# Performance work log

Hardware: AMD Instinct MI355X
Metric: run time of the kernel (lower is better)

Reference implementation:

```python
import jax, jax.numpy as jnp
import numpy as np

B, SEQ, S, DIM_IN, DIM_K, DIM_V = 4, 2048, 128, 512, 64, 64
L = SEQ + 2 * S
NEG = -1e30  # stand-in for log(0) in the tril mask (finite for stable vjp)


def _layernorm(x, g, b, eps=1e-5):
    m = jnp.mean(x, axis=-1, keepdims=True)
    v = jnp.var(x, axis=-1, keepdims=True)
    return (x - m) / jnp.sqrt(v + eps) * g + b


def setup_inputs() -> dict:
    key = jax.random.key(0)
    ks = jax.random.split(key, 18)
    w = lambda k, shape, s=0.02: (jax.random.normal(k, shape, jnp.float32) * s)
    inp = {
        "x": jax.random.normal(ks[0], (B, L, DIM_IN), jnp.float32),
        "Wq": w(ks[1], (DIM_IN, DIM_K)),
        "Wk": w(ks[2], (DIM_IN, DIM_K)),
        "Wv": w(ks[3], (DIM_IN, DIM_V)),
        "Wq_s": w(ks[4], (DIM_IN, DIM_K)),
        "Wk_s": w(ks[5], (DIM_IN, DIM_K)),
        "Wv_s": w(ks[6], (DIM_IN, DIM_V)),
        "Wq_e": w(ks[7], (DIM_IN, DIM_K)),
        "Wk_e": w(ks[8], (DIM_IN, DIM_K)),
        "Wv_e": w(ks[9], (DIM_IN, DIM_V)),
        "ln_g": jnp.ones((DIM_IN,), jnp.float32),
        "ln_b": jnp.zeros((DIM_IN,), jnp.float32),
        "ln_s_g": jnp.ones((DIM_IN,), jnp.float32),
        "ln_s_b": jnp.zeros((DIM_IN,), jnp.float32),
        "ln_e_g": jnp.ones((DIM_IN,), jnp.float32),
        "ln_e_b": jnp.zeros((DIM_IN,), jnp.float32),
        "cope_emb": jax.random.normal(ks[10], (DIM_K, S), jnp.float32),
        "offset": 0,
    }
    return inp


def reference(x, Wq, Wk, Wv, Wq_s, Wk_s, Wv_s, Wq_e, Wk_e, Wv_e,
              ln_g, ln_b, ln_s_g, ln_s_b, ln_e_g, ln_e_b, cope_emb, offset):
    # extract_state: first/last state_len tokens
    xs, xm, xe = x[:, :S], x[:, S:L - S], x[:, -S:]
    xm = _layernorm(xm, ln_g, ln_b)
    xs = _layernorm(xs, ln_s_g, ln_s_b)
    xe = _layernorm(xe, ln_e_g, ln_e_b)

    q, k, v = xm @ Wq, xm @ Wk, xm @ Wv          # (B, SEQ, dk/dv)
    q_s, k_s, v_s = xs @ Wq_s, xs @ Wk_s, xs @ Wv_s
    q_e, k_e, v_e = xe @ Wq_e, xe @ Wk_e, xe @ Wv_e

    # CoPE bias over the non-state block
    logits = jnp.einsum('bqd,bkd->bqk', q, k)    # (B, SEQ, SEQ)
    gates = jax.nn.sigmoid(logits)
    pos = jnp.flip(jnp.cumsum(jnp.flip(gates, -1), axis=-1), -1)
    pos = jnp.minimum(pos, jnp.float32(S - 1))
    pos_ceil = jnp.ceil(pos).astype(jnp.int32)
    pos_floor = jnp.floor(pos).astype(jnp.int32)
    logits_int = jnp.einsum('bqd,dk->bqk', q, cope_emb)  # (B, SEQ, S)
    logits_c = jnp.take_along_axis(logits_int, pos_ceil, axis=-1)
    logits_f = jnp.take_along_axis(logits_int, pos_floor, axis=-1)
    wfrac = pos - pos_floor.astype(pos.dtype)
    bias = logits_c * wfrac + logits_f * (1.0 - wfrac)   # (B, SEQ, SEQ)

    q_full = jnp.concatenate([q_s, q, q_e], axis=1)      # (B, L, dk)
    k_full = jnp.concatenate([k_s, k, k_e], axis=1)
    v_full = jnp.concatenate([v_s, v, v_e], axis=1)

    # explicit tril log-mask bias with CoPE injected in the middle block
    tri = jnp.tril(jnp.ones((L, L), dtype=bool))
    attn_bias = jnp.where(tri, 0.0, NEG).astype(jnp.float32)
    attn_bias = jnp.broadcast_to(attn_bias, (B, L, L))
    attn_bias = attn_bias.at[:, S:L - S, S:L - S].add(bias)

    scale = 1.0 / jnp.sqrt(jnp.float32(DIM_K))
    scores = jnp.einsum('bqd,bkd->bqk', q_full, k_full) * scale + attn_bias
    att = jax.nn.softmax(scores, axis=-1)
    return jnp.einsum('bqk,bkd->bqd', att, v_full)       # (B, L, dv)
```

## Files before the change

kernel.cpp:

```cpp
#include <hip/hip_runtime.h>
#include <math.h>

#define B_    4
#define SEQ_  2048
#define S_    128
#define L_    2304
#define DIN   512
#define DK    64
#define NEGINF (-1e30f)
#define SCALE 0.125f
#define NCOLS 2176
#define NMID  8192
#define NEDGE 1024
#define LE    2304

typedef _Float16 f16;
typedef __attribute__((ext_vector_type(8))) _Float16 half8;
typedef __attribute__((ext_vector_type(4))) float f32x4;

union U4 { uint4 u; f16 h[8]; };

__global__ __launch_bounds__(256) void k_proj(
    const float* __restrict__ x,
    const float* __restrict__ Wq,  const float* __restrict__ Wk,  const float* __restrict__ Wv,
    const float* __restrict__ Wqs, const float* __restrict__ Wks, const float* __restrict__ Wvs,
    const float* __restrict__ Wqe, const float* __restrict__ Wke, const float* __restrict__ Wve,
    const float* __restrict__ g0, const float* __restrict__ b0,
    const float* __restrict__ gs, const float* __restrict__ bs,
    const float* __restrict__ ge, const float* __restrict__ be,
    f16* __restrict__ qsp, f16* __restrict__ ksp, f16* __restrict__ vhT)
{
    __shared__ f16 As[64 * 136];
    __shared__ f16 Bs[64 * 136];
    __shared__ float mean_s[64], rstd_s[64];
    const int tid  = threadIdx.x;
    const int row0 = blockIdx.x * 64;
    const int rseq = row0 % L_;
    const int seg  = (rseq < S_) ? 0 : (rseq >= L_ - S_) ? 2 : 1;
    const int m    = blockIdx.y;
    const float* W;
    if (m == 0)      W = (seg == 0) ? Wqs : (seg == 2) ? Wqe : Wq;
    else if (m == 1) W = (seg == 0) ? Wks : (seg == 2) ? Wke : Wk;
    else             W = (seg == 0) ? Wvs : (seg == 2) ? Wve : Wv;
    const float* gg = (seg == 0) ? gs : (seg == 2) ? ge : g0;
    const float* bb = (seg == 0) ? bs : (seg == 2) ? be : b0;

    {
        const int rr = tid >> 2, qq = tid & 3;
        const float4* xr = (const float4*)(x + (size_t)(row0 + rr) * DIN) + qq * 32;
        float s = 0.f, s2 = 0.f;
        #pragma unroll
        for (int i = 0; i < 32; ++i) {
            float4 v = xr[i];
            s  += v.x + v.y + v.z + v.w;
            s2 += v.x * v.x + v.y * v.y + v.z * v.z + v.w * v.w;
        }
        s  += __shfl_xor(s, 1);  s  += __shfl_xor(s, 2);
        s2 += __shfl_xor(s2, 1); s2 += __shfl_xor(s2, 2);
        if (qq == 0) {
            float mean = s * (1.f / DIN);
            mean_s[rr] = mean;
            rstd_s[rr] = rsqrtf(s2 * (1.f / DIN) - mean * mean + 1e-5f);
        }
    }

    const int w = tid >> 6, lane = tid & 63;
    const int cl = lane & 15, quad = lane >> 4;
    const int r0 = 32 * (w >> 1), c0 = 32 * (w & 1);

    f32x4 acc[2][2];
    #pragma unroll
    for (int i = 0; i < 2; ++i)
        #pragma unroll
        for (int j = 0; j < 2; ++j) acc[i][j] = 0.f;

    for (int kc = 0; kc < DIN; kc += 64) {
        __syncthreads();
        #pragma unroll
        for (int i = 0; i < 2; ++i) {
            int g = tid + 256 * i;
            int r = g >> 3, c8 = g & 7;
            const float* xp = x + (size_t)(row0 + r) * DIN + kc + c8 * 8;
            float4 a0 = *(const float4*)xp;
            float4 a1 = *(const float4*)(xp + 4);
            float4 gA = *(const float4*)(gg + kc + c8 * 8);
            float4 gB = *(const float4*)(gg + kc + c8 * 8 + 4);
            float4 bA = *(const float4*)(bb + kc + c8 * 8);
            float4 bB = *(const float4*)(bb + kc + c8 * 8 + 4);
            float mean = mean_s[r], rstd = rstd_s[r];
            float n[8];
            n[0] = (a0.x - mean) * rstd * gA.x + bA.x;
            n[1] = (a0.y - mean) * rstd * gA.y + bA.y;
            n[2] = (a0.z - mean) * rstd * gA.z + bA.z;
            n[3] = (a0.w - mean) * rstd * gA.w + bA.w;
            n[4] = (a1.x - mean) * rstd * gB.x + bB.x;
            n[5] = (a1.y - mean) * rstd * gB.y + bB.y;
            n[6] = (a1.z - mean) * rstd * gB.z + bB.z;
            n[7] = (a1.w - mean) * rstd * gB.w + bB.w;
            U4 hi, lo;
            #pragma unroll
            for (int j = 0; j < 8; ++j) {
                hi.h[j] = (f16)n[j];
                lo.h[j] = (f16)(n[j] - (float)hi.h[j]);
            }
            *(uint4*)(As + r * 136 + c8 * 8)      = hi.u;
            *(uint4*)(As + r * 136 + 64 + c8 * 8) = lo.u;
        }
        #pragma unroll
        for (int i = 0; i < 4; ++i) {
            int g = tid + 256 * i;
            int k = g >> 4, c4 = g & 15;
            float4 wv = ((const float4*)W)[(size_t)(kc + k) * 16 + c4];
            f16 h0 = (f16)wv.x, h1 = (f16)wv.y, h2 = (f16)wv.z, h3 = (f16)wv.w;
            Bs[(c4 * 4 + 0) * 136 + k] = h0;
            Bs[(c4 * 4 + 1) * 136 + k] = h1;
            Bs[(c4 * 4 + 2) * 136 + k] = h2;
            Bs[(c4 * 4 + 3) * 136 + k] = h3;
            Bs[(c4 * 4 + 0) * 136 + 64 + k] = (f16)(wv.x - (float)h0);
            Bs[(c4 * 4 + 1) * 136 + 64 + k] = (f16)(wv.y - (float)h1);
            Bs[(c4 * 4 + 2) * 136 + 64 + k] = (f16)(wv.z - (float)h2);
            Bs[(c4 * 4 + 3) * 136 + 64 + k] = (f16)(wv.w - (float)h3);
        }
        __syncthreads();
        #pragma unroll
        for (int h = 0; h < 2; ++h) {
            half8 ah[2], al[2], bh[2], bl[2];
            #pragma unroll
            for (int rs = 0; rs < 2; ++rs) {
                const f16* base = As + (r0 + 16 * rs + cl) * 136 + h * 32 + quad * 8;
                ah[rs] = *(const half8*)(base);
                al[rs] = *(const half8*)(base + 64);
            }
            #pragma unroll
            for (int cs = 0; cs < 2; ++cs) {
                const f16* base = Bs + (c0 + 16 * cs + cl) * 136 + h * 32 + quad * 8;
                bh[cs] = *(const half8*)(base);
                bl[cs] = *(const half8*)(base + 64);
            }
            #pragma unroll
            for (int rs = 0; rs < 2; ++rs)
                #pragma unroll
                for (int cs = 0; cs < 2; ++cs) {
                    acc[rs][cs] = __builtin_amdgcn_mfma_f32_16x16x32_f16(ah[rs], bh[cs], acc[rs][cs], 0, 0, 0);
                    if (m < 2) {
                        acc[rs][cs] = __builtin_amdgcn_mfma_f32_16x16x32_f16(ah[rs], bl[cs], acc[rs][cs], 0, 0, 0);
                        acc[rs][cs] = __builtin_amdgcn_mfma_f32_16x16x32_f16(al[rs], bh[cs], acc[rs][cs], 0, 0, 0);
                    }
                }
        }
    }

    const int bI = row0 / L_;
    const int rb = row0 - bI * L_;
    f16* sp = (m == 0) ? qsp : ksp;
    #pragma unroll
    for (int rs = 0; rs < 2; ++rs)
        #pragma unroll
        for (int cs = 0; cs < 2; ++cs)
            #pragma unroll
            for (int r = 0; r < 4; ++r) {
                int lrow = r0 + 16 * rs + quad * 4 + r;
                int col  = c0 + 16 * cs + cl;
                float v  = acc[rs][cs][r];
                size_t grow = (size_t)(row0 + lrow);
                if (m < 2) {
                    f16 hv = (f16)v;
                    sp[grow * 128 + col]      = hv;
                    sp[grow * 128 + 64 + col] = (f16)(v - (float)hv);
                } else {
                    vhT[(size_t)(bI * 64 + col) * L_ + rb + lrow] = (f16)v;
                }
            }
}

__global__ __launch_bounds__(256) void k_dots(
    const f16* __restrict__ qsp, const f16* __restrict__ ksp,
    f16* __restrict__ D, float* __restrict__ G, f16* __restrict__ De)
{
    const int bx = blockIdx.x, by = blockIdx.y;
    const bool edge = (bx >= 64);
    int b, q0 = 0;
    size_t qrow0;
    if (!edge) {
        if (by >= 34) return;
        b = bx >> 4;
        q0 = (bx * 128) & 2047;
        qrow0 = (size_t)b * L_ + S_ + q0;
    } else {
        int ex = bx - 64;
        b = ex >> 1;
        int half = ex & 1;
        if (half == 0 && by > 1) return;
        qrow0 = (size_t)b * L_ + (half ? 2176 : 0);
    }
    const int col0 = by * 64;
    const size_t krow0 = (size_t)b * L_ + col0;

    __shared__ f16 Qs[128 * 136];
    __shared__ f16 Ks[64 * 136];
    const int tid = threadIdx.x;

    #pragma unroll
    for (int i = 0; i < 8; ++i) {
        int g = tid + 256 * i;
        int r = g >> 4, c = g & 15;
        *(uint4*)(Qs + r * 136 + c * 8) = *(const uint4*)(qsp + (qrow0 + r) * 128 + c * 8);
    }
    #pragma unroll
    for (int i = 0; i < 4; ++i) {
        int g = tid + 256 * i;
        int r = g >> 4, c = g & 15;
        *(uint4*)(Ks + r * 136 + c * 8) = *(const uint4*)(ksp + (krow0 + r) * 128 + c * 8);
    }
    __syncthreads();

    const int w = tid >> 6, lane = tid & 63;
    const int cl = lane & 15, quad = lane >> 4;

    f32x4 acc[2][4];
    #pragma unroll
    for (int i = 0; i < 2; ++i)
        #pragma unroll
        for (int j = 0; j < 4; ++j) acc[i][j] = 0.f;

    #pragma unroll
    for (int h = 0; h < 2; ++h) {
        half8 ah[2], al[2], bh[4], bl[4];
        #pragma unroll
        for (int rs = 0; rs < 2; ++rs) {
            const f16* base = Qs + (32 * w + 16 * rs + cl) * 136 + h * 32 + quad * 8;
            ah[rs] = *(const half8*)(base);
            al[rs] = *(const half8*)(base + 64);
        }
        #pragma unroll
        for (int c = 0; c < 4; ++c) {
            const f16* base = Ks + (16 * c + cl) * 136 + h * 32 + quad * 8;
            bh[c] = *(const half8*)(base);
            bl[c] = *(const half8*)(base + 64);
        }
        #pragma unroll
        for (int rs = 0; rs < 2; ++rs)
            #pragma unroll
            for (int c = 0; c < 4; ++c) {
                acc[rs][c] = __builtin_amdgcn_mfma_f32_16x16x32_f16(ah[rs], bh[c], acc[rs][c], 0, 0, 0);
                acc[rs][c] = __builtin_amdgcn_mfma_f32_16x16x32_f16(ah[rs], bl[c], acc[rs][c], 0, 0, 0);
                acc[rs][c] = __builtin_amdgcn_mfma_f32_16x16x32_f16(al[rs], bh[c], acc[rs][c], 0, 0, 0);
            }
    }

    if (!edge) {
        const int gr0 = bx * 128;
        const bool writeD = (by < 2) || ((by - 2) <= (q0 >> 6) + 1);
        if (writeD) {
            #pragma unroll
            for (int rs = 0; rs < 2; ++rs)
                #pragma unroll
                for (int c = 0; c < 4; ++c)
                    #pragma unroll
                    for (int r = 0; r < 4; ++r) {
                        int mrow = gr0 + 32 * w + 16 * rs + quad * 4 + r;
                        int n    = col0 + 16 * c + cl;
                        D[(size_t)mrow * NCOLS + n] = (f16)acc[rs][c][r];
                    }
        }
        if (by >= 2) {
            const int chm = by - 2;
            #pragma unroll
            for (int rs = 0; rs < 2; ++rs)
                #pragma unroll
                for (int r = 0; r < 4; ++r) {
                    float s = 0.f;
                    #pragma unroll
                    for (int c = 0; c < 4; ++c)
                        s += 1.f / (1.f + __expf(-acc[rs][c][r]));
                    #pragma unroll
                    for (int off = 1; off < 16; off <<= 1) s += __shfl_xor(s, off);
                    if (cl == 0)
                        G[(size_t)(gr0 + 32 * w + 16 * rs + quad * 4 + r) * 32 + chm] = s;
                }
        }
    } else {
        const int er0 = (bx - 64) * 128;
        #pragma unroll
        for (int rs = 0; rs < 2; ++rs)
            #pragma unroll
            for (int c = 0; c < 4; ++c)
                #pragma unroll
                for (int r = 0; r < 4; ++r) {
                    int erow = er0 + 32 * w + 16 * rs + quad * 4 + r;
                    int n    = col0 + 16 * c + cl;
                    De[(size_t)erow * LE + n] = (f16)acc[rs][c][r];
                }
    }
}

__global__ __launch_bounds__(256) void k_scan(
    const f16* __restrict__ qsp, const float* __restrict__ cope,
    const float* __restrict__ G, f16* __restrict__ D, f16* __restrict__ De)
{
    __shared__ f16   qvh[128];
    __shared__ float li[128];
    __shared__ float Gs[32];
    __shared__ float Gsf[32];
    __shared__ float wmax[4], wsum[4];
    const int tid = threadIdx.x;
    const int gr  = blockIdx.x;
    const int lane = tid & 63, wid = tid >> 6;

    if (gr < NMID) {
        const int b = gr >> 11;
        const int q = gr & 2047;
        const size_t grow = (size_t)b * L_ + S_ + q;
        const int qlim = (q & ~63) + 64;

        if (tid < 16) ((uint4*)qvh)[tid] = ((const uint4*)(qsp + grow * 128))[tid];
        if (tid >= 16 && tid < 24)
            ((float4*)Gs)[tid - 16] = ((const float4*)G)[(size_t)gr * 8 + tid - 16];
        __syncthreads();
        if (tid < 128) {
            float a = 0.f;
            #pragma unroll
            for (int d = 0; d < DK; ++d)
                a += ((float)qvh[d] + (float)qvh[64 + d]) * cope[d * S_ + tid];
            li[tid] = a;
        }
        if (tid >= 128 && tid < 160) {
            int c = tid - 128;
            float s = 0.f;
            for (int cc = c + 1; cc < 32; ++cc) s += Gs[cc];
            Gsf[c] = s;
        }

        f16* Dr = D + (size_t)gr * NCOLS;
        const int j0 = tid * 8;
        const int cg = tid >> 3, sl = tid & 7;
        float dot[8], gte[8];
        float csum = 0.f;
        if (j0 < qlim) {
            U4 t; t.u = *(const uint4*)(Dr + 128 + j0);
            #pragma unroll
            for (int jj = 0; jj < 8; ++jj) {
                dot[jj] = (float)t.h[jj];
                gte[jj] = 1.f / (1.f + __expf(-dot[jj]));
                csum += gte[jj];
            }
        } else {
            #pragma unroll
            for (int jj = 0; jj < 8; ++jj) { dot[jj] = 0.f; gte[jj] = 0.f; }
        }
        float sv = (tid < 128) ? (float)Dr[tid] * SCALE : NEGINF;

        float inc = csum;
        #pragma unroll
        for (int off = 1; off < 8; off <<= 1) {
            float u = __shfl_down(inc, off, 8);
            if (sl + off < 8) inc += u;
        }
        __syncthreads();
        float run = (inc - csum) + Gsf[cg];

        float p8[8];
        #pragma unroll
        for (int jj = 7; jj >= 0; --jj) {
            run += gte[jj];
            float pos = fminf(run, (float)(S_ - 1));
            float pfl = floorf(pos);
            int ic  = (int)ceilf(pos);
            int ifl = (int)pfl;
            float w = pos - pfl;
            float bias = li[ic] * w + li[ifl] * (1.f - w);
            p8[jj] = (j0 + jj <= q) ? dot[jj] * SCALE + bias : NEGINF;
        }

        float mx = sv;
        #pragma unroll
        for (int jj = 0; jj < 8; ++jj) mx = fmaxf(mx, p8[jj]);
        #pragma unroll
        for (int off = 1; off < 64; off <<= 1) mx = fmaxf(mx, __shfl_xor(mx, off));
        if (lane == 0) wmax[wid] = mx;
        __syncthreads();
        mx = fmaxf(fmaxf(wmax[0], wmax[1]), fmaxf(wmax[2], wmax[3]));

        float lsum = 0.f;
        float e8[8];
        #pragma unroll
        for (int jj = 0; jj < 8; ++jj) {
            e8[jj] = __expf(p8[jj] - mx);
            lsum += e8[jj];
        }
        float es = 0.f;
        if (tid < 128) { es = __expf(sv - mx); lsum += es; }
        #pragma unroll
        for (int off = 1; off < 64; off <<= 1) lsum += __shfl_xor(lsum, off);
        if (lane == 0) wsum[wid] = lsum;
        __syncthreads();
        float inv = 1.f / (wsum[0] + wsum[1] + wsum[2] + wsum[3]);

        if (j0 < qlim) {
            U4 o;
            #pragma unroll
            for (int jj = 0; jj < 8; ++jj) o.h[jj] = (f16)(e8[jj] * inv);
            *(uint4*)(Dr + 128 + j0) = o.u;
        }
        if (tid < 128) Dr[tid] = (f16)(es * inv);
    } else {
        const int er = gr - NMID;
        const int r  = er & 255;
        const int Q  = (r < 128) ? r : (2048 + r);
        f16* Er = De + (size_t)er * LE;

        float v[9];
        #pragma unroll
        for (int i = 0; i < 9; ++i) {
            int j = tid + 256 * i;
            float d = (float)Er[j];
            v[i] = (j <= Q) ? d * SCALE : NEGINF;
        }
        float mx = v[0];
        #pragma unroll
        for (int i = 1; i < 9; ++i) mx = fmaxf(mx, v[i]);
        #pragma unroll
        for (int off = 1; off < 64; off <<= 1) mx = fmaxf(mx, __shfl_xor(mx, off));
        if (lane == 0) wmax[wid] = mx;
        __syncthreads();
        mx = fmaxf(fmaxf(wmax[0], wmax[1]), fmaxf(wmax[2], wmax[3]));

        float lsum = 0.f;
        #pragma unroll
        for (int i = 0; i < 9; ++i) {
            v[i] = __expf(v[i] - mx);
            lsum += v[i];
        }
        #pragma unroll
        for (int off = 1; off < 64; off <<= 1) lsum += __shfl_xor(lsum, off);
        if (lane == 0) wsum[wid] = lsum;
        __syncthreads();
        float inv = 1.f / (wsum[0] + wsum[1] + wsum[2] + wsum[3]);

        #pragma unroll
        for (int i = 0; i < 9; ++i)
            Er[tid + 256 * i] = (f16)(v[i] * inv);
    }
}

__global__ __launch_bounds__(256) void k_pv(
    const f16* __restrict__ Pmid, const f16* __restrict__ Pedge,
    const f16* __restrict__ vhT, float* __restrict__ out)
{
    __shared__ f16 Ps[64 * 72];
    __shared__ f16 Vt[64 * 72];
    const int tid = threadIdx.x;
    const int bx  = blockIdx.x;
    const int ks  = blockIdx.y;
    const bool edge = (bx >= 128);

    const f16* Pb;
    size_t pitch;
    int row0, b, cap, cmax;
    if (!edge) {
        row0 = bx * 64;
        b = row0 >> 11;
        int q0 = row0 & 2047;
        Pb = Pmid; pitch = NCOLS; cap = 34;
        cmax = (191 + q0) >> 6;
    } else {
        row0 = (bx - 128) * 64;
        b = row0 >> 8;
        int r0 = row0 & 255;
        Pb = Pedge; pitch = LE; cap = 36;
        int Qmax = (r0 < 128) ? (r0 + 63) : (2048 + r0 + 63);
        cmax = Qmax >> 6;
    }
    const int c_beg = ks * 9;
    int c_end = c_beg + 9;
    if (c_end > cap) c_end = cap;
    if (c_end > cmax + 1) c_end = cmax + 1;
    if (c_end <= c_beg) return;

    const int w = tid >> 6, lane = tid & 63;
    const int cl = lane & 15, quad = lane >> 4;
    f32x4 acc[4];
    #pragma unroll
    for (int c = 0; c < 4; ++c) acc[c] = 0.f;

    for (int ch = c_beg; ch < c_end; ++ch) {
        __syncthreads();
        #pragma unroll
        for (int i = 0; i < 2; ++i) {
            int g = tid + 256 * i;
            int r = g >> 3, c = g & 7;
            *(uint4*)(Ps + r * 72 + c * 8) =
                *(const uint4*)(Pb + (size_t)(row0 + r) * pitch + ch * 64 + c * 8);
            *(uint4*)(Vt + r * 72 + c * 8) =
                *(const uint4*)(vhT + (size_t)(b * 64 + r) * L_ + ch * 64 + c * 8);
        }
        __syncthreads();
        #pragma unroll
        for (int h = 0; h < 2; ++h) {
            half8 a = *(const half8*)(Ps + (16 * w + cl) * 72 + h * 32 + quad * 8);
            #pragma unroll
            for (int c = 0; c < 4; ++c) {
                half8 bv = *(const half8*)(Vt + (16 * c + cl) * 72 + h * 32 + quad * 8);
                acc[c] = __builtin_amdgcn_mfma_f32_16x16x32_f16(a, bv, acc[c], 0, 0, 0);
            }
        }
    }
    #pragma unroll
    for (int c = 0; c < 4; ++c)
        #pragma unroll
        for (int r = 0; r < 4; ++r) {
            int lrow = row0 + 16 * w + quad * 4 + r;
            int n    = 16 * c + cl;
            size_t orow;
            if (!edge) {
                orow = (size_t)b * L_ + S_ + (lrow & 2047);
            } else {
                int rr = lrow & 255;
                int gQ = (rr < 128) ? rr : (2048 + rr);
                orow = (size_t)b * L_ + gQ;
            }
            atomicAdd(&out[orow * DK + n], acc[c][r]);
        }
}

extern "C" void kernel_launch(void* const* d_in, const int* in_sizes, int n_in,
                              void* d_out, int out_size, void* d_ws, size_t ws_size,
                              hipStream_t stream)
{
    const float* x    = (const float*)d_in[0];
    const float* Wq   = (const float*)d_in[1];
    const float* Wk   = (const float*)d_in[2];
    const float* Wv   = (const float*)d_in[3];
    const float* Wqs  = (const float*)d_in[4];
    const float* Wks  = (const float*)d_in[5];
    const float* Wvs  = (const float*)d_in[6];
    const float* Wqe  = (const float*)d_in[7];
    const float* Wke  = (const float*)d_in[8];
    const float* Wve  = (const float*)d_in[9];
    const float* g0   = (const float*)d_in[10];
    const float* b0   = (const float*)d_in[11];
    const float* gs   = (const float*)d_in[12];
    const float* bs   = (const float*)d_in[13];
    const float* ge   = (const float*)d_in[14];
    const float* be   = (const float*)d_in[15];
    const float* cope = (const float*)d_in[16];

    const size_t NR = (size_t)B_ * L_;
    f16*   qsp = (f16*)d_ws;
    f16*   ksp = qsp + NR * 128;
    f16*   vhT = ksp + NR * 128;
    float* G   = (float*)(vhT + NR * 64);
    f16*   D   = (f16*)(G + (size_t)NMID * 32);
    f16*   De  = D + (size_t)NMID * NCOLS;
    float* out = (float*)d_out;

    hipMemsetAsync(out, 0, (size_t)out_size * sizeof(float), stream);
    k_proj<<<dim3(144, 3), 256, 0, stream>>>(x, Wq, Wk, Wv, Wqs, Wks, Wvs,
                                             Wqe, Wke, Wve, g0, b0, gs, bs,
                                             ge, be, qsp, ksp, vhT);
    k_dots<<<dim3(72, 36), 256, 0, stream>>>(qsp, ksp, D, G, De);
    k_scan<<<NMID + NEDGE, 256, 0, stream>>>(qsp, cope, G, D, De);
    k_pv  <<<dim3(144, 4), 256, 0, stream>>>(D, De, vhT, out);
}
```

Measured before the change: 199.2 us.

## Presplit weights, widen dots tile, replace PV atomics with partial-sum merge

Adds a kernel that converts and transposes each weight matrix into hi/lo fp16 pairs once, so the projection blocks stop redoing that conversion with scattered LDS stores. The dots kernel now computes 128-column key tiles instead of 64, halving the number of blocks and Q reloads, and emits two gate-sum chunks per block. The PV kernel writes per-split partial outputs to a workspace and a new merge kernel sums them, replacing the memset and the float atomics. This costs two extra launches, more workspace traffic, and more accumulator registers in the dots kernel.

Result: faster. 192.5 us (-3.4%).

```diff
diff --git a/kernel.cpp b/kernel.cpp
--- a/kernel.cpp
+++ b/kernel.cpp
@@ -20,11 +20,49 @@
 
 union U4 { uint4 u; f16 h[8]; };
 
-__global__ __launch_bounds__(256) void k_proj(
-    const float* __restrict__ x,
+__global__ __launch_bounds__(256) void k_wsplit(
     const float* __restrict__ Wq,  const float* __restrict__ Wk,  const float* __restrict__ Wv,
     const float* __restrict__ Wqs, const float* __restrict__ Wks, const float* __restrict__ Wvs,
     const float* __restrict__ Wqe, const float* __restrict__ Wke, const float* __restrict__ Wve,
+    f16* __restrict__ Wsp)
+{
+    __shared__ float xs[64 * 68];
+    const int kt  = blockIdx.x;
+    const int mat = blockIdx.y;
+    const float* W;
+    switch (mat) {
+        case 0: W = Wq;  break; case 1: W = Wk;  break; case 2: W = Wv;  break;
+        case 3: W = Wqs; break; case 4: W = Wks; break; case 5: W = Wvs; break;
+        case 6: W = Wqe; break; case 7: W = Wke; break; default: W = Wve; break;
+    }
+    const int tid = threadIdx.x;
+    const int k0  = kt * 64;
+    #pragma unroll
+    for (int i = 0; i < 4; ++i) {
+        int g = tid + 256 * i;
+        int k = g >> 4, c4 = g & 15;
+        *(float4*)(xs + k * 68 + c4 * 4) = ((const float4*)W)[(size_t)(k0 + k) * 16 + c4];
+    }
+    __syncthreads();
+    const int col = tid & 63, hf = tid >> 6;
+    const int kk0 = hf * 16;
+    U4 hi0, hi1, lo0, lo1;
+    #pragma unroll
+    for (int j = 0; j < 8; ++j) {
+        float v0 = xs[(kk0 + j) * 68 + col];
+        float v1 = xs[(kk0 + 8 + j) * 68 + col];
+        hi0.h[j] = (f16)v0; lo0.h[j] = (f16)(v0 - (float)hi0.h[j]);
+        hi1.h[j] = (f16)v1; lo1.h[j] = (f16)(v1 - (float)hi1.h[j]);
+    }
+    f16* dst = Wsp + (size_t)mat * 65536 + (size_t)col * 1024 + k0 + kk0;
+    *(uint4*)(dst)       = hi0.u;
+    *(uint4*)(dst + 8)   = hi1.u;
+    *(uint4*)(dst + 512) = lo0.u;
+    *(uint4*)(dst + 520) = lo1.u;
+}
+
+__global__ __launch_bounds__(256) void k_proj(
+    const float* __restrict__ x, const f16* __restrict__ Wsp,
     const float* __restrict__ g0, const float* __restrict__ b0,
     const float* __restrict__ gs, const float* __restrict__ bs,
     const float* __restrict__ ge, const float* __restrict__ be,
@@ -38,10 +76,8 @@
     const int rseq = row0 % L_;
     const int seg  = (rseq < S_) ? 0 : (rseq >= L_ - S_) ? 2 : 1;
     const int m    = blockIdx.y;
-    const float* W;
-    if (m == 0)      W = (seg == 0) ? Wqs : (seg == 2) ? Wqe : Wq;
-    else if (m == 1) W = (seg == 0) ? Wks : (seg == 2) ? Wke : Wk;
-    else             W = (seg == 0) ? Wvs : (seg == 2) ? Wve : Wv;
+    const int mat  = m + ((seg == 0) ? 3 : (seg == 2) ? 6 : 0);
+    const f16* Wc  = Wsp + (size_t)mat * 65536;
     const float* gg = (seg == 0) ? gs : (seg == 2) ? ge : g0;
     const float* bb = (seg == 0) ? bs : (seg == 2) ? be : b0;
 
@@ -107,19 +143,12 @@
             *(uint4*)(As + r * 136 + 64 + c8 * 8) = lo.u;
         }
         #pragma unroll
-        for (int i = 0; i < 4; ++i) {
+        for (int i = 0; i < 2; ++i) {
             int g = tid + 256 * i;
-            int k = g >> 4, c4 = g & 15;
-            float4 wv = ((const float4*)W)[(size_t)(kc + k) * 16 + c4];
-            f16 h0 = (f16)wv.x, h1 = (f16)wv.y, h2 = (f16)wv.z, h3 = (f16)wv.w;
-            Bs[(c4 * 4 + 0) * 136 + k] = h0;
-            Bs[(c4 * 4 + 1) * 136 + k] = h1;
-            Bs[(c4 * 4 + 2) * 136 + k] = h2;
-            Bs[(c4 * 4 + 3) * 136 + k] = h3;
-            Bs[(c4 * 4 + 0) * 136 + 64 + k] = (f16)(wv.x - (float)h0);
-            Bs[(c4 * 4 + 1) * 136 + 64 + k] = (f16)(wv.y - (float)h1);
-            Bs[(c4 * 4 + 2) * 136 + 64 + k] = (f16)(wv.z - (float)h2);
-            Bs[(c4 * 4 + 3) * 136 + 64 + k] = (f16)(wv.w - (float)h3);
+            int col = g >> 3, c8 = g & 7;
+            const f16* src = Wc + (size_t)col * 1024 + kc + c8 * 8;
+            *(uint4*)(Bs + col * 136 + c8 * 8)      = *(const uint4*)(src);
+            *(uint4*)(Bs + col * 136 + 64 + c8 * 8) = *(const uint4*)(src + 512);
         }
         __syncthreads();
         #pragma unroll
@@ -182,7 +211,7 @@
     int b, q0 = 0;
     size_t qrow0;
     if (!edge) {
-        if (by >= 34) return;
+        if (by >= 17) return;
         b = bx >> 4;
         q0 = (bx * 128) & 2047;
         qrow0 = (size_t)b * L_ + S_ + q0;
@@ -190,14 +219,14 @@
         int ex = bx - 64;
         b = ex >> 1;
         int half = ex & 1;
-        if (half == 0 && by > 1) return;
+        if (half == 0 && by > 0) return;
         qrow0 = (size_t)b * L_ + (half ? 2176 : 0);
     }
-    const int col0 = by * 64;
+    const int col0 = by * 128;
     const size_t krow0 = (size_t)b * L_ + col0;
 
     __shared__ f16 Qs[128 * 136];
-    __shared__ f16 Ks[64 * 136];
+    __shared__ f16 Ks[128 * 136];
     const int tid = threadIdx.x;
 
     #pragma unroll
@@ -205,11 +234,6 @@
         int g = tid + 256 * i;
         int r = g >> 4, c = g & 15;
         *(uint4*)(Qs + r * 136 + c * 8) = *(const uint4*)(qsp + (qrow0 + r) * 128 + c * 8);
-    }
-    #pragma unroll
-    for (int i = 0; i < 4; ++i) {
-        int g = tid + 256 * i;
-        int r = g >> 4, c = g & 15;
         *(uint4*)(Ks + r * 136 + c * 8) = *(const uint4*)(ksp + (krow0 + r) * 128 + c * 8);
     }
     __syncthreads();
@@ -217,15 +241,15 @@
     const int w = tid >> 6, lane = tid & 63;
     const int cl = lane & 15, quad = lane >> 4;
 
-    f32x4 acc[2][4];
+    f32x4 acc[2][8];
     #pragma unroll
     for (int i = 0; i < 2; ++i)
         #pragma unroll
-        for (int j = 0; j < 4; ++j) acc[i][j] = 0.f;
+        for (int j = 0; j < 8; ++j) acc[i][j] = 0.f;
 
     #pragma unroll
     for (int h = 0; h < 2; ++h) {
-        half8 ah[2], al[2], bh[4], bl[4];
+        half8 ah[2], al[2];
         #pragma unroll
         for (int rs = 0; rs < 2; ++rs) {
             const f16* base = Qs + (32 * w + 16 * rs + cl) * 136 + h * 32 + quad * 8;
@@ -233,29 +257,34 @@
             al[rs] = *(const half8*)(base + 64);
         }
         #pragma unroll
-        for (int c = 0; c < 4; ++c) {
-            const f16* base = Ks + (16 * c + cl) * 136 + h * 32 + quad * 8;
-            bh[c] = *(const half8*)(base);
-            bl[c] = *(const half8*)(base + 64);
-        }
-        #pragma unroll
-        for (int rs = 0; rs < 2; ++rs)
-            #pragma unroll
-            for (int c = 0; c < 4; ++c) {
-                acc[rs][c] = __builtin_amdgcn_mfma_f32_16x16x32_f16(ah[rs], bh[c], acc[rs][c], 0, 0, 0);
-                acc[rs][c] = __builtin_amdgcn_mfma_f32_16x16x32_f16(ah[rs], bl[c], acc[rs][c], 0, 0, 0);
-                acc[rs][c] = __builtin_amdgcn_mfma_f32_16x16x32_f16(al[rs], bh[c], acc[rs][c], 0, 0, 0);
+        for (int cq = 0; cq < 2; ++cq) {
+            half8 bh[4], bl[4];
+            #pragma unroll
+            for (int cc = 0; cc < 4; ++cc) {
+                const f16* base = Ks + (16 * (cq * 4 + cc) + cl) * 136 + h * 32 + quad * 8;
+                bh[cc] = *(const half8*)(base);
+                bl[cc] = *(const half8*)(base + 64);
             }
+            #pragma unroll
+            for (int rs = 0; rs < 2; ++rs)
+                #pragma unroll
+                for (int cc = 0; cc < 4; ++cc) {
+                    int c = cq * 4 + cc;
+                    acc[rs][c] = __builtin_amdgcn_mfma_f32_16x16x32_f16(ah[rs], bh[cc], acc[rs][c], 0, 0, 0);
+                    acc[rs][c] = __builtin_amdgcn_mfma_f32_16x16x32_f16(ah[rs], bl[cc], acc[rs][c], 0, 0, 0);
+                    acc[rs][c] = __builtin_amdgcn_mfma_f32_16x16x32_f16(al[rs], bh[cc], acc[rs][c], 0, 0, 0);
+                }
+        }
     }
 
     if (!edge) {
         const int gr0 = bx * 128;
-        const bool writeD = (by < 2) || ((by - 2) <= (q0 >> 6) + 1);
+        const bool writeD = (by == 0) || ((by - 1) <= (q0 >> 7));
         if (writeD) {
             #pragma unroll
             for (int rs = 0; rs < 2; ++rs)
                 #pragma unroll
-                for (int c = 0; c < 4; ++c)
+                for (int c = 0; c < 8; ++c)
                     #pragma unroll
                     for (int r = 0; r < 4; ++r) {
                         int mrow = gr0 + 32 * w + 16 * rs + quad * 4 + r;
@@ -263,20 +292,28 @@
                         D[(size_t)mrow * NCOLS + n] = (f16)acc[rs][c][r];
                     }
         }
-        if (by >= 2) {
-            const int chm = by - 2;
+        if (by >= 1) {
+            const int chm = 2 * (by - 1);
             #pragma unroll
             for (int rs = 0; rs < 2; ++rs)
                 #pragma unroll
                 for (int r = 0; r < 4; ++r) {
-                    float s = 0.f;
+                    float sA = 0.f, sB = 0.f;
                     #pragma unroll
-                    for (int c = 0; c < 4; ++c)
-                        s += 1.f / (1.f + __expf(-acc[rs][c][r]));
+                    for (int cc = 0; cc < 4; ++cc) {
+                        sA += 1.f / (1.f + __expf(-acc[rs][cc][r]));
+                        sB += 1.f / (1.f + __expf(-acc[rs][4 + cc][r]));
+                    }
                     #pragma unroll
-                    for (int off = 1; off < 16; off <<= 1) s += __shfl_xor(s, off);
-                    if (cl == 0)
-                        G[(size_t)(gr0 + 32 * w + 16 * rs + quad * 4 + r) * 32 + chm] = s;
+                    for (int off = 1; off < 16; off <<= 1) {
+                        sA += __shfl_xor(sA, off);
+                        sB += __shfl_xor(sB, off);
+                    }
+                    if (cl == 0) {
+                        int row = gr0 + 32 * w + 16 * rs + quad * 4 + r;
+                        G[(size_t)row * 32 + chm]     = sA;
+                        G[(size_t)row * 32 + chm + 1] = sB;
+                    }
                 }
         }
     } else {
@@ -284,7 +321,7 @@
         #pragma unroll
         for (int rs = 0; rs < 2; ++rs)
             #pragma unroll
-            for (int c = 0; c < 4; ++c)
+            for (int c = 0; c < 8; ++c)
                 #pragma unroll
                 for (int r = 0; r < 4; ++r) {
                     int erow = er0 + 32 * w + 16 * rs + quad * 4 + r;
@@ -445,7 +482,8 @@
 
 __global__ __launch_bounds__(256) void k_pv(
     const f16* __restrict__ Pmid, const f16* __restrict__ Pedge,
-    const f16* __restrict__ vhT, float* __restrict__ out)
+    const f16* __restrict__ vhT,
+    float* __restrict__ Opart, float* __restrict__ Oe)
 {
     __shared__ f16 Ps[64 * 72];
     __shared__ f16 Vt[64 * 72];
@@ -457,12 +495,14 @@
     const f16* Pb;
     size_t pitch;
     int row0, b, cap, cmax;
+    float* outp;
     if (!edge) {
         row0 = bx * 64;
         b = row0 >> 11;
         int q0 = row0 & 2047;
         Pb = Pmid; pitch = NCOLS; cap = 34;
         cmax = (191 + q0) >> 6;
+        outp = Opart + (size_t)ks * NMID * DK;
     } else {
         row0 = (bx - 128) * 64;
         b = row0 >> 8;
@@ -470,12 +510,12 @@
         Pb = Pedge; pitch = LE; cap = 36;
         int Qmax = (r0 < 128) ? (r0 + 63) : (2048 + r0 + 63);
         cmax = Qmax >> 6;
+        outp = Oe + (size_t)ks * NEDGE * DK;
     }
     const int c_beg = ks * 9;
     int c_end = c_beg + 9;
     if (c_end > cap) c_end = cap;
     if (c_end > cmax + 1) c_end = cmax + 1;
-    if (c_end <= c_beg) return;
 
     const int w = tid >> 6, lane = tid & 63;
     const int cl = lane & 15, quad = lane >> 4;
@@ -509,18 +549,32 @@
     for (int c = 0; c < 4; ++c)
         #pragma unroll
         for (int r = 0; r < 4; ++r) {
-            int lrow = row0 + 16 * w + quad * 4 + r;
+            int mrow = row0 + 16 * w + quad * 4 + r;
             int n    = 16 * c + cl;
-            size_t orow;
-            if (!edge) {
-                orow = (size_t)b * L_ + S_ + (lrow & 2047);
-            } else {
-                int rr = lrow & 255;
-                int gQ = (rr < 128) ? rr : (2048 + rr);
-                orow = (size_t)b * L_ + gQ;
-            }
-            atomicAdd(&out[orow * DK + n], acc[c][r]);
-        }
+            outp[(size_t)mrow * DK + n] = acc[c][r];
+        }
+}
+
+__global__ __launch_bounds__(256) void k_merge(
+    const float* __restrict__ Opart, const float* __restrict__ Oe,
+    float* __restrict__ out)
+{
+    const int e = blockIdx.x * 256 + threadIdx.x;
+    if (e < NMID * DK) {
+        const int gr = e >> 6, c = e & 63;
+        const int b  = gr >> 11, q = gr & 2047;
+        const int NP = NMID * DK;
+        float s = Opart[e] + Opart[e + NP] + Opart[e + 2 * NP] + Opart[e + 3 * NP];
+        out[((size_t)b * L_ + S_ + q) * DK + c] = s;
+    } else {
+        const int e2 = e - NMID * DK;
+        const int er = e2 >> 6, c = e2 & 63;
+        const int b  = er >> 8, r = er & 255;
+        const int gQ = (r < 128) ? r : (2048 + r);
+        const int NP = NEDGE * DK;
+        float s = Oe[e2] + Oe[e2 + NP] + Oe[e2 + 2 * NP] + Oe[e2 + 3 * NP];
+        out[((size_t)b * L_ + gQ) * DK + c] = s;
+    }
 }
 
 extern "C" void kernel_launch(void* const* d_in, const int* in_sizes, int n_in,
@@ -546,19 +600,23 @@
     const float* cope = (const float*)d_in[16];
 
     const size_t NR = (size_t)B_ * L_;
-    f16*   qsp = (f16*)d_ws;
-    f16*   ksp = qsp + NR * 128;
-    f16*   vhT = ksp + NR * 128;
-    float* G   = (float*)(vhT + NR * 64);
-    f16*   D   = (f16*)(G + (size_t)NMID * 32);
-    f16*   De  = D + (size_t)NMID * NCOLS;
-    float* out = (float*)d_out;
-
-    hipMemsetAsync(out, 0, (size_t)out_size * sizeof(float), stream);
-    k_proj<<<dim3(144, 3), 256, 0, stream>>>(x, Wq, Wk, Wv, Wqs, Wks, Wvs,
-                                             Wqe, Wke, Wve, g0, b0, gs, bs,
-                                             ge, be, qsp, ksp, vhT);
-    k_dots<<<dim3(72, 36), 256, 0, stream>>>(qsp, ksp, D, G, De);
+    f16*   qsp   = (f16*)d_ws;
+    f16*   ksp   = qsp + NR * 128;
+    f16*   vhT   = ksp + NR * 128;
+    f16*   Wsp   = vhT + NR * 64;
+    float* G     = (float*)(Wsp + (size_t)9 * 65536);
+    float* Opart = G + (size_t)NMID * 32;
+    float* Oe    = Opart + (size_t)4 * NMID * DK;
+    f16*   D     = (f16*)(Oe + (size_t)4 * NEDGE * DK);
+    f16*   De    = D + (size_t)NMID * NCOLS;
+    float* out   = (float*)d_out;
+
+    k_wsplit<<<dim3(8, 9), 256, 0, stream>>>(Wq, Wk, Wv, Wqs, Wks, Wvs,
+                                             Wqe, Wke, Wve, Wsp);
+    k_proj<<<dim3(144, 3), 256, 0, stream>>>(x, Wsp, g0, b0, gs, bs, ge, be,
+                                             qsp, ksp, vhT);
+    k_dots<<<dim3(72, 18), 256, 0, stream>>>(qsp, ksp, D, G, De);
     k_scan<<<NMID + NEDGE, 256, 0, stream>>>(qsp, cope, G, D, De);
-    k_pv  <<<dim3(144, 4), 256, 0, stream>>>(D, De, vhT, out);
+    k_pv  <<<dim3(144, 4), 256, 0, stream>>>(D, De, vhT, Opart, Oe);
+    k_merge<<<(NMID + NEDGE) * DK / 256, 256, 0, stream>>>(Opart, Oe, out);
 }
```
